# Kernel optimization log

Hardware: AMD Instinct MI355X
Metric: run time of the kernel (lower is better)

## Reference

```python
import jax, jax.numpy as jnp
import numpy as np

N_NODES = 50000


def gcn_conv(x, W, b, src, dst, n):
    """PyG GCNConv: add self-loops, symmetric deg^-1/2 normalization, then aggregate."""
    loop = jnp.arange(n, dtype=src.dtype)
    s = jnp.concatenate([src, loop])  # [E+N]
    d = jnp.concatenate([dst, loop])  # [E+N]
    deg = jax.ops.segment_sum(jnp.ones_like(d, dtype=x.dtype), d, num_segments=n)  # [N]
    dinv = jnp.where(deg > 0, jax.lax.rsqrt(deg), 0.0)
    h = x @ W  # transform first (reduces message width), [N, out]
    norm = (dinv[s] * dinv[d])[:, None]  # [E+N, 1]
    msgs = h[s] * norm  # gather + scale, [E+N, out]
    out = jax.ops.segment_sum(msgs, d, num_segments=n)  # scatter-add, [N, out]
    return out + b


def setup_inputs() -> dict:
    key = jax.random.key(0)
    k1, k2, k3, k4 = jax.random.split(key, 4)
    in_dim, hidden, n_cls = 512, 256, 64
    x = jax.random.normal(k1, (N_NODES, in_dim), dtype=jnp.float32)
    edge_index = jax.random.randint(k2, (2, 800000), 0, N_NODES, dtype=jnp.int64)
    W1 = jax.random.normal(k3, (in_dim, hidden), dtype=jnp.float32) / np.sqrt(in_dim)
    b1 = jnp.zeros((hidden,), dtype=jnp.float32)
    W2 = jax.random.normal(k4, (hidden, n_cls), dtype=jnp.float32) / np.sqrt(hidden)
    b2 = jnp.zeros((n_cls,), dtype=jnp.float32)
    return {"x": x, "edge_index": edge_index, "W1": W1, "b1": b1, "W2": W2, "b2": b2}


def reference(x, edge_index, W1, b1, W2, b2):
    src, dst = edge_index[0], edge_index[1]
    n = x.shape[0]
    h = jax.nn.relu(gcn_conv(x, W1, b1, src, dst, n))  # dropout is identity in eval mode
    logits = gcn_conv(h, W2, b2, src, dst, n)
    evidence = jax.nn.softplus(logits)
    return (evidence, h)
```

## Files before the change

### kernel.cpp

```cpp
#include <hip/hip_runtime.h>


#define N_NODES 50000
#define IN_DIM 512
#define HID 256
#define NCLS 64

typedef unsigned short u16;
typedef unsigned int u32;
typedef __attribute__((ext_vector_type(8))) short short8;
typedef __attribute__((ext_vector_type(4))) float float4_t;

__device__ __forceinline__ float bf_lo(u32 v) {
    u32 u = v << 16; float f; __builtin_memcpy(&f, &u, 4); return f;
}
__device__ __forceinline__ float bf_hi(u32 v) {
    u32 u = v & 0xffff0000u; float f; __builtin_memcpy(&f, &u, 4); return f;
}
__device__ __forceinline__ u16 f2bf(float f) {
    u32 u; __builtin_memcpy(&u, &f, 4);
    return (u16)((u + 0x7fffu + ((u >> 16) & 1u)) >> 16);
}
__device__ __forceinline__ u32 pack2bf(float a, float b) {
    return (u32)f2bf(a) | ((u32)f2bf(b) << 16);
}
__device__ __forceinline__ void add8(float* acc, uint4 v) {
    acc[0] += bf_lo(v.x); acc[1] += bf_hi(v.x);
    acc[2] += bf_lo(v.y); acc[3] += bf_hi(v.y);
    acc[4] += bf_lo(v.z); acc[5] += bf_hi(v.z);
    acc[6] += bf_lo(v.w); acc[7] += bf_hi(v.w);
}
__device__ __forceinline__ void acc8(float* acc, uint4 v, float w) {
    acc[0] += w * bf_lo(v.x); acc[1] += w * bf_hi(v.x);
    acc[2] += w * bf_lo(v.y); acc[3] += w * bf_hi(v.y);
    acc[4] += w * bf_lo(v.z); acc[5] += w * bf_hi(v.z);
    acc[6] += w * bf_lo(v.w); acc[7] += w * bf_hi(v.w);
}

__global__ void init_kernel(int* __restrict__ cnt, int* __restrict__ cursor, int n) {
    int i = blockIdx.x * blockDim.x + threadIdx.x;
    if (i < n) { cnt[i] = 0; cursor[i] = 0; }
}

__global__ void count_kernel(const int* __restrict__ dst, int* __restrict__ cnt, int E) {
    int e = blockIdx.x * blockDim.x + threadIdx.x;
    if (e < E) atomicAdd(&cnt[dst[e]], 1);
}

__global__ __launch_bounds__(256) void s1_kernel(const int* __restrict__ cnt,
                                                 int* __restrict__ blocksum,
                                                 float* __restrict__ dinv, int n) {
    int tid = threadIdx.x;
    int i = blockIdx.x * 256 + tid;
    int c = (i < n) ? cnt[i] : 0;
    if (i < n) dinv[i] = rsqrtf((float)(c + 1));
    __shared__ int s[256];
    s[tid] = c;
    __syncthreads();
    for (int off = 128; off > 0; off >>= 1) {
        if (tid < off) s[tid] += s[tid + off];
        __syncthreads();
    }
    if (tid == 0) blocksum[blockIdx.x] = s[0];
}

__global__ __launch_bounds__(256) void s3_kernel(const int* __restrict__ cnt,
                                                 const int* __restrict__ blocksum,
                                                 int* __restrict__ row_ptr, int n, int nb) {
    __shared__ int bs[256];
    __shared__ int s[256];
    int tid = threadIdx.x;
    int v = (tid < nb) ? blocksum[tid] : 0;
    bs[tid] = v;
    __syncthreads();
    for (int off = 1; off < 256; off <<= 1) {
        int a = (tid >= off) ? bs[tid - off] : 0;
        __syncthreads();
        bs[tid] += a;
        __syncthreads();
    }
    int boff = (blockIdx.x == 0) ? 0 : bs[blockIdx.x - 1];
    int i = blockIdx.x * 256 + tid;
    int c = (i < n) ? cnt[i] : 0;
    s[tid] = c;
    __syncthreads();
    for (int off = 1; off < 256; off <<= 1) {
        int a = (tid >= off) ? s[tid - off] : 0;
        __syncthreads();
        s[tid] += a;
        __syncthreads();
    }
    if (i <= n) row_ptr[i] = boff + s[tid] - c;
}

__global__ void fill_kernel(const int* __restrict__ src, const int* __restrict__ dst,
                            const int* __restrict__ row_ptr, int* __restrict__ cursor,
                            int* __restrict__ csr_src, int E) {
    int e = blockIdx.x * blockDim.x + threadIdx.x;
    if (e >= E) return;
    int d = dst[e];
    int pos = row_ptr[d] + atomicAdd(&cursor[d], 1);
    csr_src[pos] = src[e];
}

__global__ __launch_bounds__(256) void tcast_kernel(const float* __restrict__ W,
                                                    u16* __restrict__ Wt, int K, int N) {
    int idx = blockIdx.x * 256 + threadIdx.x;
    if (idx >= K * N) return;
    int n = idx / K, k = idx - n * K;
    Wt[idx] = f2bf(W[k * N + n]);
}

template <int BM, int BN, int K, int N, bool AF32, bool SCALE>
__global__ __launch_bounds__(256) void mfma_gemm_kernel(const void* __restrict__ Ain,
                                                        const u16* __restrict__ Bt,
                                                        u16* __restrict__ C, int M,
                                                        const float* __restrict__ rowscale) {
    constexpr int WROWS = 2, WCOLS = 2;
    constexpr int WMR = BM / WROWS;
    constexpr int WNR = BN / WCOLS;
    constexpr int MR = WMR / 16;
    constexpr int NR = WNR / 16;
    constexpr int AI = BM / 64;
    constexpr int BI = BN / 64;
    constexpr int LDSA = BM * 32;
    constexpr int LDSB = BN * 32;
    constexpr int LDST = LDSA + LDSB;
    constexpr int NT = K / 32;
    static_assert(MR * 16 * WROWS == BM && NR * 16 * WCOLS == BN, "tiling");
    __shared__ u16 lds[2 * LDST];

    const int tid = threadIdx.x;
    const int wave = tid >> 6, lane = tid & 63;
    const int wm = wave / WCOLS, wn = wave % WCOLS;
    const int quad = lane >> 4, l15 = lane & 15;
    const int row0 = blockIdx.y * BM;
    const int col0 = blockIdx.x * BN;

    const float* Af = (const float*)Ain;
    const u16* Abf = (const u16*)Ain;

    int gra[AI];
#pragma unroll
    for (int i = 0; i < AI; i++) {
        int gr = row0 + ((tid + i * 256) >> 2);
        gra[i] = gr < M ? gr : M - 1;
    }

    float4 pa[AI][2];

    auto loadA = [&](int k0) {
#pragma unroll
        for (int i = 0; i < AI; i++) {
            int c = tid + i * 256;
            const float* gp = Af + (long)gra[i] * K + k0 + (c & 3) * 8;
            pa[i][0] = ((const float4*)gp)[0];
            pa[i][1] = ((const float4*)gp)[1];
        }
    };
    auto writeA = [&](u16* buf) {
#pragma unroll
        for (int i = 0; i < AI; i++) {
            int c = tid + i * 256;
            uint4 o;
            o.x = pack2bf(pa[i][0].x, pa[i][0].y);
            o.y = pack2bf(pa[i][0].z, pa[i][0].w);
            o.z = pack2bf(pa[i][1].x, pa[i][1].y);
            o.w = pack2bf(pa[i][1].z, pa[i][1].w);
            *(uint4*)(buf + c * 8) = o;
        }
    };
    auto stageA_lds = [&](int k0, u16* buf) {
#pragma unroll
        for (int i = 0; i < AI; i++) {
            int c = tid + i * 256;
            const u16* gp = Abf + (long)gra[i] * K + k0 + (c & 3) * 8;
            __builtin_amdgcn_global_load_lds((const __attribute__((address_space(1))) u32*)gp,
                                             (__attribute__((address_space(3))) u32*)(buf + c * 8),
                                             16, 0, 0);
        }
    };
    auto stageB = [&](int k0, u16* buf) {
#pragma unroll
        for (int i = 0; i < BI; i++) {
            int c = tid + i * 256;
            int r = c >> 2;
            const u16* gp = Bt + (long)(col0 + r) * K + k0 + (c & 3) * 8;
            __builtin_amdgcn_global_load_lds((const __attribute__((address_space(1))) u32*)gp,
                                             (__attribute__((address_space(3))) u32*)(buf + c * 8),
                                             16, 0, 0);
        }
    };

    float4_t acc[MR][NR];
#pragma unroll
    for (int mi = 0; mi < MR; mi++)
#pragma unroll
        for (int ni = 0; ni < NR; ni++) {
            float4_t z = {0.f, 0.f, 0.f, 0.f};
            acc[mi][ni] = z;
        }

    if constexpr (AF32) {
        loadA(0);
        writeA(lds);
    } else {
        stageA_lds(0, lds);
    }
    stageB(0, lds + LDSA);
    __syncthreads();

    for (int t = 0; t < NT; t++) {
        u16* cur = lds + (t & 1) * LDST;
        u16* nxt = lds + ((t + 1) & 1) * LDST;
        const bool pre = (t + 1) < NT;
        if (pre) {
            if constexpr (AF32) loadA((t + 1) * 32);
            else stageA_lds((t + 1) * 32, nxt);
            stageB((t + 1) * 32, nxt + LDSA);
        }

        short8 af[MR], bfr[NR];
#pragma unroll
        for (int mi = 0; mi < MR; mi++)
            af[mi] = *(const short8*)(cur + (wm * WMR + mi * 16 + l15) * 32 + quad * 8);
#pragma unroll
        for (int ni = 0; ni < NR; ni++)
            bfr[ni] = *(const short8*)(cur + LDSA + (wn * WNR + ni * 16 + l15) * 32 + quad * 8);
#pragma unroll
        for (int mi = 0; mi < MR; mi++)
#pragma unroll
            for (int ni = 0; ni < NR; ni++)
                acc[mi][ni] = __builtin_amdgcn_mfma_f32_16x16x32_bf16(af[mi], bfr[ni],
                                                                      acc[mi][ni], 0, 0, 0);
        if (pre) {
            if constexpr (AF32) writeA(nxt);
        }
        __syncthreads();
    }

#pragma unroll
    for (int mi = 0; mi < MR; mi++) {
#pragma unroll
        for (int r = 0; r < 4; r++) {
            int row = row0 + wm * WMR + mi * 16 + quad * 4 + r;
            if (row < M) {
                float sc = 1.f;
                if constexpr (SCALE) sc = rowscale[row];
#pragma unroll
                for (int ni = 0; ni < NR; ni++) {
                    int col = col0 + wn * WNR + ni * 16 + l15;
                    C[(long)row * N + col] = f2bf(acc[mi][ni][r] * sc);
                }
            }
        }
    }
}

__global__ __launch_bounds__(256) void agg_wide_kernel(const u16* __restrict__ t,
                                                       const int* __restrict__ row_ptr,
                                                       const int* __restrict__ csr_src,
                                                       const float* __restrict__ dinv,
                                                       const float* __restrict__ bias,
                                                       float* __restrict__ out_f,
                                                       u16* __restrict__ out_bf, int n) {
    constexpr int FEAT = 256;
    int node = (blockIdx.x * blockDim.x + threadIdx.x) >> 6;
    int lane = threadIdx.x & 63;
    if (node >= n) return;
    const int g = lane >> 5;
    const int r = lane & 31;
    float acc[8] = {};
    const int beg = row_ptr[node], end = row_ptr[node + 1];
    int e = beg;
    for (; e + 16 <= end; e += 16) {
        int s[8]; uint4 v[8];
#pragma unroll
        for (int u = 0; u < 8; u++) s[u] = csr_src[e + u * 2 + g];
#pragma unroll
        for (int u = 0; u < 8; u++) v[u] = *(const uint4*)(t + (long)s[u] * FEAT + r * 8);
#pragma unroll
        for (int u = 0; u < 8; u++) add8(acc, v[u]);
    }
    for (; e + 8 <= end; e += 8) {
        int s[4]; uint4 v[4];
#pragma unroll
        for (int u = 0; u < 4; u++) s[u] = csr_src[e + u * 2 + g];
#pragma unroll
        for (int u = 0; u < 4; u++) v[u] = *(const uint4*)(t + (long)s[u] * FEAT + r * 8);
#pragma unroll
        for (int u = 0; u < 4; u++) add8(acc, v[u]);
    }
    for (; e < end; e += 2) {
        int ee = e + g;
        if (ee < end) {
            int s = csr_src[ee];
            uint4 v = *(const uint4*)(t + (long)s * FEAT + r * 8);
            add8(acc, v);
        }
    }
#pragma unroll
    for (int j = 0; j < 8; j++) acc[j] += __shfl_xor(acc[j], 32, 64);

    if (lane < 32) {
        const float di = dinv[node];
        uint4 sv = *(const uint4*)(t + (long)node * FEAT + lane * 8);
        float self[8] = {bf_lo(sv.x), bf_hi(sv.x), bf_lo(sv.y), bf_hi(sv.y),
                         bf_lo(sv.z), bf_hi(sv.z), bf_lo(sv.w), bf_hi(sv.w)};
        float4 b0 = *(const float4*)(bias + lane * 8);
        float4 b1 = *(const float4*)(bias + lane * 8 + 4);
        float bb[8] = {b0.x, b0.y, b0.z, b0.w, b1.x, b1.y, b1.z, b1.w};
        float rv[8];
#pragma unroll
        for (int j = 0; j < 8; j++)
            rv[j] = fmaxf(di * (acc[j] + self[j]) + bb[j], 0.f);
        long base = (long)node * FEAT + lane * 8;
        *(float4*)(out_f + base) = make_float4(rv[0], rv[1], rv[2], rv[3]);
        *(float4*)(out_f + base + 4) = make_float4(rv[4], rv[5], rv[6], rv[7]);
        uint4 o;
        o.x = (u32)f2bf(rv[0]) | ((u32)f2bf(rv[1]) << 16);
        o.y = (u32)f2bf(rv[2]) | ((u32)f2bf(rv[3]) << 16);
        o.z = (u32)f2bf(rv[4]) | ((u32)f2bf(rv[5]) << 16);
        o.w = (u32)f2bf(rv[6]) | ((u32)f2bf(rv[7]) << 16);
        *(uint4*)(out_bf + base) = o;
    }
}

__global__ __launch_bounds__(256) void agg_n8_kernel(const u16* __restrict__ t,
                                                     const int* __restrict__ row_ptr,
                                                     const int* __restrict__ csr_src,
                                                     const float* __restrict__ dinv,
                                                     const float* __restrict__ bias,
                                                     float* __restrict__ out_f, int n) {
    constexpr int FEAT = 64;
    const int wid = (blockIdx.x * blockDim.x + threadIdx.x) >> 6;
    const int lane = threadIdx.x & 63;
    const int g = lane >> 3;
    const int r = lane & 7;
    const int node = wid * 8 + g;
    const bool valid = node < n;
    const int nd = valid ? node : (n - 1);
    const int beg = row_ptr[nd];
    const int deg = valid ? (row_ptr[nd + 1] - beg) : 0;
    float acc[8] = {};
    for (int e = 0;; e += 4) {
        if (!__any(e < deg)) break;
        int s[4]; float w[4]; uint4 v[4];
#pragma unroll
        for (int u = 0; u < 4; u++) {
            bool a = (e + u) < deg;
            s[u] = a ? csr_src[beg + e + u] : 0;
            w[u] = a ? 1.f : 0.f;
        }
#pragma unroll
        for (int u = 0; u < 4; u++) v[u] = *(const uint4*)(t + (long)s[u] * FEAT + r * 8);
#pragma unroll
        for (int u = 0; u < 4; u++) acc8(acc, v[u], w[u]);
    }
    const float di = dinv[nd];
    uint4 sv = *(const uint4*)(t + (long)nd * FEAT + r * 8);
    float self[8] = {bf_lo(sv.x), bf_hi(sv.x), bf_lo(sv.y), bf_hi(sv.y),
                     bf_lo(sv.z), bf_hi(sv.z), bf_lo(sv.w), bf_hi(sv.w)};
    float4 b0 = *(const float4*)(bias + r * 8);
    float4 b1 = *(const float4*)(bias + r * 8 + 4);
    float bb[8] = {b0.x, b0.y, b0.z, b0.w, b1.x, b1.y, b1.z, b1.w};
    float rv[8];
#pragma unroll
    for (int j = 0; j < 8; j++) {
        float v = di * (acc[j] + self[j]) + bb[j];
        rv[j] = fmaxf(v, 0.f) + __logf(1.f + __expf(-fabsf(v)));
    }
    if (valid) {
        long base = (long)nd * FEAT + r * 8;
        *(float4*)(out_f + base) = make_float4(rv[0], rv[1], rv[2], rv[3]);
        *(float4*)(out_f + base + 4) = make_float4(rv[4], rv[5], rv[6], rv[7]);
    }
}

extern "C" void kernel_launch(void* const* d_in, const int* in_sizes, int n_in,
                              void* d_out, int out_size, void* d_ws, size_t ws_size,
                              hipStream_t stream) {
    const float* x  = (const float*)d_in[0];
    const int*   ei = (const int*)d_in[1];
    const float* W1 = (const float*)d_in[2];
    const float* b1 = (const float*)d_in[3];
    const float* W2 = (const float*)d_in[4];
    const float* b2 = (const float*)d_in[5];

    float* evidence = (float*)d_out;
    float* h        = (float*)d_out + (long)N_NODES * NCLS;

    const int E = in_sizes[1] / 2;
    const int* src = ei;
    const int* dst = ei + E;

    const int NB = (N_NODES + 255) / 256;

    char* w = (char*)d_ws;
    int*   cnt      = (int*)w;  w += 50048 * 4;
    int*   cursor   = (int*)w;  w += 50048 * 4;
    int*   row_ptr  = (int*)w;  w += 50064 * 4;
    float* dinv     = (float*)w; w += 50048 * 4;
    int*   blocksum = (int*)w;  w += 256 * 4;
    int*   csr_src  = (int*)w;  w += 800000 * 4;
    u16*   hbf      = (u16*)w;  w += (long)N_NODES * IN_DIM * 2;
    u16*   w1t      = (u16*)w;  w += IN_DIM * HID * 2;
    u16*   w2t      = (u16*)w;  w += HID * NCLS * 2;
    u16*   t1bf     = (u16*)w;  w += (long)N_NODES * HID * 2;
    u16*   t2bf     = t1bf;

    init_kernel<<<NB, 256, 0, stream>>>(cnt, cursor, N_NODES);
    count_kernel<<<(E + 255) / 256, 256, 0, stream>>>(dst, cnt, E);
    s1_kernel<<<NB, 256, 0, stream>>>(cnt, blocksum, dinv, N_NODES);
    s3_kernel<<<NB, 256, 0, stream>>>(cnt, blocksum, row_ptr, N_NODES, NB);
    fill_kernel<<<(E + 255) / 256, 256, 0, stream>>>(src, dst, row_ptr, cursor, csr_src, E);

    tcast_kernel<<<(IN_DIM * HID + 255) / 256, 256, 0, stream>>>(W1, w1t, IN_DIM, HID);
    tcast_kernel<<<(HID * NCLS + 255) / 256, 256, 0, stream>>>(W2, w2t, HID, NCLS);

    {
        dim3 grid(HID / 128, (N_NODES + 127) / 128);
        mfma_gemm_kernel<128, 128, IN_DIM, HID, true, true>
            <<<grid, 256, 0, stream>>>(x, w1t, t1bf, N_NODES, dinv);
    }
    agg_wide_kernel<<<(N_NODES * 64 + 255) / 256, 256, 0, stream>>>(
        t1bf, row_ptr, csr_src, dinv, b1, h, hbf, N_NODES);

    {
        dim3 grid(NCLS / 64, (N_NODES + 63) / 64);
        mfma_gemm_kernel<64, 64, HID, NCLS, false, true>
            <<<grid, 256, 0, stream>>>(hbf, w2t, t2bf, N_NODES, dinv);
    }
    {
        int waves = (N_NODES + 7) / 8;
        int blocks = (waves + 3) / 4;
        agg_n8_kernel<<<blocks, 256, 0, stream>>>(
            t2bf, row_ptr, csr_src, dinv, b2, evidence, N_NODES);
    }
}
```

Baseline: 396.3 us.

## Use hardware bf16 pack, nontemporal stores, merged weight cast, and narrower GEMM tile

Replaces the software bf16 rounding with the v_cvt_pk_bf16_f32 instruction in the GEMM A-staging and in the aggregation output. Output stores of h and evidence become nontemporal, and the self-row, dinv and bias loads are hoisted ahead of the edge loop so their latency overlaps with it. The two weight transpose-cast launches are merged into one. The first GEMM's tile drops from 128x128 to 128x64, doubling the grid to 4x391 blocks but reloading each A tile twice.

```diff
diff --git a/kernel.cpp b/kernel.cpp
--- a/kernel.cpp
+++ b/kernel.cpp
@@ -21,8 +21,10 @@
     u32 u; __builtin_memcpy(&u, &f, 4);
     return (u16)((u + 0x7fffu + ((u >> 16) & 1u)) >> 16);
 }
-__device__ __forceinline__ u32 pack2bf(float a, float b) {
-    return (u32)f2bf(a) | ((u32)f2bf(b) << 16);
+__device__ __forceinline__ u32 pk_bf16(float lo, float hi) {
+    u32 r;
+    asm("v_cvt_pk_bf16_f32 %0, %1, %2" : "=v"(r) : "v"(lo), "v"(hi));
+    return r;
 }
 __device__ __forceinline__ void add8(float* acc, uint4 v) {
     acc[0] += bf_lo(v.x); acc[1] += bf_hi(v.x);
@@ -35,6 +37,10 @@
     acc[2] += w * bf_lo(v.y); acc[3] += w * bf_hi(v.y);
     acc[4] += w * bf_lo(v.z); acc[5] += w * bf_hi(v.z);
     acc[6] += w * bf_lo(v.w); acc[7] += w * bf_hi(v.w);
+}
+__device__ __forceinline__ void nt_store4(float* p, float a, float b, float c, float d) {
+    float4_t v = {a, b, c, d};
+    __builtin_nontemporal_store(v, (float4_t*)p);
 }
 
 __global__ void init_kernel(int* __restrict__ cnt, int* __restrict__ cursor, int n) {
@@ -103,12 +109,22 @@
     csr_src[pos] = src[e];
 }
 
-__global__ __launch_bounds__(256) void tcast_kernel(const float* __restrict__ W,
-                                                    u16* __restrict__ Wt, int K, int N) {
+__global__ __launch_bounds__(256) void tcast2_kernel(const float* __restrict__ W1,
+                                                     u16* __restrict__ W1t,
+                                                     const float* __restrict__ W2,
+                                                     u16* __restrict__ W2t) {
     int idx = blockIdx.x * 256 + threadIdx.x;
-    if (idx >= K * N) return;
-    int n = idx / K, k = idx - n * K;
-    Wt[idx] = f2bf(W[k * N + n]);
+    constexpr int N1 = IN_DIM * HID;
+    if (idx < N1) {
+        int n = idx / IN_DIM, k = idx - n * IN_DIM;
+        W1t[idx] = f2bf(W1[k * HID + n]);
+    } else {
+        int j = idx - N1;
+        if (j < HID * NCLS) {
+            int n = j / HID, k = j - n * HID;
+            W2t[j] = f2bf(W2[k * NCLS + n]);
+        }
+    }
 }
 
 template <int BM, int BN, int K, int N, bool AF32, bool SCALE>
@@ -163,10 +179,10 @@
         for (int i = 0; i < AI; i++) {
             int c = tid + i * 256;
             uint4 o;
-            o.x = pack2bf(pa[i][0].x, pa[i][0].y);
-            o.y = pack2bf(pa[i][0].z, pa[i][0].w);
-            o.z = pack2bf(pa[i][1].x, pa[i][1].y);
-            o.w = pack2bf(pa[i][1].z, pa[i][1].w);
+            o.x = pk_bf16(pa[i][0].x, pa[i][0].y);
+            o.y = pk_bf16(pa[i][0].z, pa[i][0].w);
+            o.z = pk_bf16(pa[i][1].x, pa[i][1].y);
+            o.w = pk_bf16(pa[i][1].z, pa[i][1].w);
             *(uint4*)(buf + c * 8) = o;
         }
     };
@@ -270,6 +286,12 @@
     if (node >= n) return;
     const int g = lane >> 5;
     const int r = lane & 31;
+
+    const float di = dinv[node];
+    uint4 sv = *(const uint4*)(t + (long)node * FEAT + r * 8);
+    float4 b0 = *(const float4*)(bias + r * 8);
+    float4 b1 = *(const float4*)(bias + r * 8 + 4);
+
     float acc[8] = {};
     const int beg = row_ptr[node], end = row_ptr[node + 1];
     int e = beg;
@@ -303,25 +325,21 @@
     for (int j = 0; j < 8; j++) acc[j] += __shfl_xor(acc[j], 32, 64);
 
     if (lane < 32) {
-        const float di = dinv[node];
-        uint4 sv = *(const uint4*)(t + (long)node * FEAT + lane * 8);
         float self[8] = {bf_lo(sv.x), bf_hi(sv.x), bf_lo(sv.y), bf_hi(sv.y),
                          bf_lo(sv.z), bf_hi(sv.z), bf_lo(sv.w), bf_hi(sv.w)};
-        float4 b0 = *(const float4*)(bias + lane * 8);
-        float4 b1 = *(const float4*)(bias + lane * 8 + 4);
         float bb[8] = {b0.x, b0.y, b0.z, b0.w, b1.x, b1.y, b1.z, b1.w};
         float rv[8];
 #pragma unroll
         for (int j = 0; j < 8; j++)
             rv[j] = fmaxf(di * (acc[j] + self[j]) + bb[j], 0.f);
         long base = (long)node * FEAT + lane * 8;
-        *(float4*)(out_f + base) = make_float4(rv[0], rv[1], rv[2], rv[3]);
-        *(float4*)(out_f + base + 4) = make_float4(rv[4], rv[5], rv[6], rv[7]);
+        nt_store4(out_f + base, rv[0], rv[1], rv[2], rv[3]);
+        nt_store4(out_f + base + 4, rv[4], rv[5], rv[6], rv[7]);
         uint4 o;
-        o.x = (u32)f2bf(rv[0]) | ((u32)f2bf(rv[1]) << 16);
-        o.y = (u32)f2bf(rv[2]) | ((u32)f2bf(rv[3]) << 16);
-        o.z = (u32)f2bf(rv[4]) | ((u32)f2bf(rv[5]) << 16);
-        o.w = (u32)f2bf(rv[6]) | ((u32)f2bf(rv[7]) << 16);
+        o.x = pk_bf16(rv[0], rv[1]);
+        o.y = pk_bf16(rv[2], rv[3]);
+        o.z = pk_bf16(rv[4], rv[5]);
+        o.w = pk_bf16(rv[6], rv[7]);
         *(uint4*)(out_bf + base) = o;
     }
 }
@@ -342,6 +360,12 @@
     const int nd = valid ? node : (n - 1);
     const int beg = row_ptr[nd];
     const int deg = valid ? (row_ptr[nd + 1] - beg) : 0;
+
+    const float di = dinv[nd];
+    uint4 sv = *(const uint4*)(t + (long)nd * FEAT + r * 8);
+    float4 b0 = *(const float4*)(bias + r * 8);
+    float4 b1 = *(const float4*)(bias + r * 8 + 4);
+
     float acc[8] = {};
     for (int e = 0;; e += 4) {
         if (!__any(e < deg)) break;
@@ -357,12 +381,8 @@
 #pragma unroll
         for (int u = 0; u < 4; u++) acc8(acc, v[u], w[u]);
     }
-    const float di = dinv[nd];
-    uint4 sv = *(const uint4*)(t + (long)nd * FEAT + r * 8);
     float self[8] = {bf_lo(sv.x), bf_hi(sv.x), bf_lo(sv.y), bf_hi(sv.y),
                      bf_lo(sv.z), bf_hi(sv.z), bf_lo(sv.w), bf_hi(sv.w)};
-    float4 b0 = *(const float4*)(bias + r * 8);
-    float4 b1 = *(const float4*)(bias + r * 8 + 4);
     float bb[8] = {b0.x, b0.y, b0.z, b0.w, b1.x, b1.y, b1.z, b1.w};
     float rv[8];
 #pragma unroll
@@ -372,8 +392,8 @@
     }
     if (valid) {
         long base = (long)nd * FEAT + r * 8;
-        *(float4*)(out_f + base) = make_float4(rv[0], rv[1], rv[2], rv[3]);
-        *(float4*)(out_f + base + 4) = make_float4(rv[4], rv[5], rv[6], rv[7]);
+        nt_store4(out_f + base, rv[0], rv[1], rv[2], rv[3]);
+        nt_store4(out_f + base + 4, rv[4], rv[5], rv[6], rv[7]);
     }
 }
 
@@ -415,12 +435,14 @@
     s3_kernel<<<NB, 256, 0, stream>>>(cnt, blocksum, row_ptr, N_NODES, NB);
     fill_kernel<<<(E + 255) / 256, 256, 0, stream>>>(src, dst, row_ptr, cursor, csr_src, E);
 
-    tcast_kernel<<<(IN_DIM * HID + 255) / 256, 256, 0, stream>>>(W1, w1t, IN_DIM, HID);
-    tcast_kernel<<<(HID * NCLS + 255) / 256, 256, 0, stream>>>(W2, w2t, HID, NCLS);
-
     {
-        dim3 grid(HID / 128, (N_NODES + 127) / 128);
-        mfma_gemm_kernel<128, 128, IN_DIM, HID, true, true>
+        int tot = IN_DIM * HID + HID * NCLS;
+        tcast2_kernel<<<(tot + 255) / 256, 256, 0, stream>>>(W1, w1t, W2, w2t);
+    }
+
+    {
+        dim3 grid(HID / 64, (N_NODES + 127) / 128);
+        mfma_gemm_kernel<128, 64, IN_DIM, HID, true, true>
             <<<grid, 256, 0, stream>>>(x, w1t, t1bf, N_NODES, dinv);
     }
     agg_wide_kernel<<<(N_NODES * 64 + 255) / 256, 256, 0, stream>>>(
```

Result: no change. 397.6 us (+0.3%).
